# Kernel optimization log

Measured on AMD Instinct MI355X. Metric: run time of the kernel, lower is better.

Reference implementation:

```python
import jax, jax.numpy as jnp
import numpy as np
from jax import lax

B, S, D, H, K, FF = 8, 1024, 512, 8, 3, 1024
BUCKETS, MAX_REL = 32, 128
DH = D // H
SPAN = BUCKETS  # att_span when position_buckets > 0


def setup_inputs() -> dict:
    key = jax.random.key(0)
    ks = jax.random.split(key, 12)
    n = lambda k, shp, s=0.02: jax.random.normal(k, shp, jnp.float32) * s
    return dict(
        x=jax.random.normal(ks[0], (B, S, D), jnp.float32),
        ln1_g=jnp.ones((D,), jnp.float32), ln1_b=jnp.zeros((D,), jnp.float32),
        dw_w=n(ks[1], (D, 1, K), 0.1), dw_b=jnp.zeros((D,), jnp.float32),
        pw_w=n(ks[2], (D, D)), pw_b=jnp.zeros((D,), jnp.float32),
        ln2_g=jnp.ones((D,), jnp.float32), ln2_b=jnp.zeros((D,), jnp.float32),
        q_w=n(ks[3], (D, D)), q_b=jnp.zeros((D,), jnp.float32),
        k_w=n(ks[4], (D, D)), k_b=jnp.zeros((D,), jnp.float32),
        v_w=n(ks[5], (D, D)), v_b=jnp.zeros((D,), jnp.float32),
        o_w=n(ks[6], (D, D)), o_b=jnp.zeros((D,), jnp.float32),
        rel_emb=n(ks[7], (2 * SPAN, D)),
        ln3_g=jnp.ones((D,), jnp.float32), ln3_b=jnp.zeros((D,), jnp.float32),
        w1=n(ks[8], (FF, D)), b1=jnp.zeros((FF,), jnp.float32),
        w2=n(ks[9], (D, FF)), b2=jnp.zeros((D,), jnp.float32),
    )


def _ln(x, g, b):
    m = x.mean(-1, keepdims=True)
    v = jnp.var(x, axis=-1, keepdims=True)
    return (x - m) * lax.rsqrt(v + 1e-5) * g + b


def _rel_bucket():
    # DeBERTa-v2 log-bucket relative positions, [S, S] int32
    ids = jnp.arange(S, dtype=jnp.int32)
    rel = ids[:, None] - ids[None, :]
    mid = BUCKETS // 2
    sign = jnp.sign(rel)
    abs_pos = jnp.where((rel < mid) & (rel > -mid), mid - 1, jnp.abs(rel)).astype(jnp.float32)
    log_pos = jnp.ceil(jnp.log(abs_pos / mid) / np.log((MAX_REL - 1) / mid) * (mid - 1)) + mid
    return jnp.where(abs_pos <= mid, rel, (log_pos * sign).astype(jnp.int32)).astype(jnp.int32)


def _attention(x, q_w, q_b, k_w, k_b, v_w, v_b, o_w, o_b, rel_emb):
    def heads(t):  # [B,S,D] -> [B,H,S,DH]
        return t.reshape(B, S, H, DH).transpose(0, 2, 1, 3)

    q = heads(x @ q_w.T + q_b)
    k = heads(x @ k_w.T + k_b)
    v = heads(x @ v_w.T + v_b)
    scale = 1.0 / np.sqrt(DH * 3)  # scale_factor = 1 + len(['c2p','p2c'])

    scores = jnp.einsum('bhid,bhjd->bhij', q, k) * scale  # content-to-content

    rel = _rel_bucket()  # [S,S]
    # shared att key: project rel embeddings with same q/k projections -> [H, 2*SPAN, DH]
    pos_k = (rel_emb @ k_w.T + k_b).reshape(2 * SPAN, H, DH).transpose(1, 0, 2)
    pos_q = (rel_emb @ q_w.T + q_b).reshape(2 * SPAN, H, DH).transpose(1, 0, 2)

    # content-to-position
    c2p = jnp.einsum('bhid,hjd->bhij', q, pos_k)  # [B,H,S,2*SPAN]
    c2p_idx = jnp.clip(rel + SPAN, 0, 2 * SPAN - 1)[None, None]  # [1,1,S,S]
    scores = scores + jnp.take_along_axis(c2p, c2p_idx, axis=-1) * scale

    # position-to-content
    p2c = jnp.einsum('bhid,hjd->bhij', k, pos_q)  # [B,H,S,2*SPAN]
    p2c_idx = jnp.clip(-rel + SPAN, 0, 2 * SPAN - 1)[None, None]
    scores = scores + jnp.take_along_axis(p2c, p2c_idx, axis=-1).swapaxes(-1, -2) * scale

    probs = jax.nn.softmax(scores, axis=-1)
    ctx = jnp.einsum('bhij,bhjd->bhid', probs, v).transpose(0, 2, 1, 3).reshape(B, S, D)
    return ctx @ o_w.T + o_b


def reference(x, ln1_g, ln1_b, dw_w, dw_b, pw_w, pw_b, ln2_g, ln2_b,
              q_w, q_b, k_w, k_b, v_w, v_b, o_w, o_b, rel_emb,
              ln3_g, ln3_b, w1, b1, w2, b2):
    # conv block (pre-norm)
    res = x
    xn = _ln(x, ln1_g, ln1_b)
    xc = xn.transpose(0, 2, 1)  # [B,D,S]
    dw = lax.conv_general_dilated(xc, dw_w, (1,), [(K // 2, K // 2)],
                                  dimension_numbers=('NCH', 'OIH', 'NCH'),
                                  feature_group_count=D) + dw_b[None, :, None]
    pw = jnp.einsum('od,bds->bos', pw_w, jax.nn.silu(dw)) + pw_b[None, :, None]
    x = res + pw.transpose(0, 2, 1)
    # attention block
    res = x
    x = res + _attention(_ln(x, ln2_g, ln2_b), q_w, q_b, k_w, k_b, v_w, v_b, o_w, o_b, rel_emb)
    # FFN block
    res = x
    xn = _ln(x, ln3_g, ln3_b)
    ff = jax.nn.silu(xn @ w1.T + b1) @ w2.T + b2
    return res + ff
```

## Files before the change

kernel.cpp:

```cpp
#include <hip/hip_runtime.h>
#include <hip/hip_bf16.h>
#include <math.h>


#define B_  8
#define S_  1024
#define D_  512
#define H_  8
#define DH_ 64
#define FF_ 1024
#define BS_ (B_*S_)
#define SCALE_ 0.07216878364f

typedef __attribute__((ext_vector_type(8))) short  short8;
typedef __attribute__((ext_vector_type(4))) short  short4v;
typedef __attribute__((ext_vector_type(4))) float  f32x4;
typedef __attribute__((ext_vector_type(4))) int    int4v;

static __device__ __forceinline__ float b2f(short u){
  union { int i; float f; } cv; cv.i = ((int)(unsigned short)u) << 16; return cv.f;
}
static __device__ __forceinline__ short f2b(float f){
  union { float f; unsigned u; } cv; cv.f = f;
  unsigned r = cv.u + 0x7FFFu + ((cv.u >> 16) & 1u);
  return (short)(r >> 16);
}
static __device__ __forceinline__ float silu_f(float x){
  return x / (1.f + __expf(-x));
}
static __device__ __forceinline__ f32x4 mfma16(short8 a, short8 b, f32x4 c){
  return __builtin_amdgcn_mfma_f32_16x16x32_bf16(a, b, c, 0, 0, 0);
}
static __device__ __forceinline__ void gl16(const void* g, void* l){
  __builtin_amdgcn_global_load_lds((const __attribute__((address_space(1))) void*)g,
                                   (__attribute__((address_space(3))) void*)l, 16, 0, 0);
}

struct F2B8 { const float* s[8]; short* d[8]; int n[8]; };
__global__ __launch_bounds__(256) void f2b8_kernel(F2B8 a){
  int seg = blockIdx.y;
  int i = (blockIdx.x*256 + threadIdx.x)*4;
  if (i >= a.n[seg]) return;
  float4 v = *(const float4*)(a.s[seg] + i);
  short4v o; o.x = f2b(v.x); o.y = f2b(v.y); o.z = f2b(v.z); o.w = f2b(v.w);
  *(short4v*)(a.d[seg] + i) = o;
}

__global__ __launch_bounds__(256) void tab_kernel(signed char* __restrict__ tab){
  int t = blockIdx.x*256 + threadIdx.x;
  if (t >= 2048) return;
  int d = t - 1023;
  int ad = d < 0 ? -d : d;
  int bkt;
  if (ad <= 16) bkt = d;
  else {
    const float inv_log = 15.f / logf(7.9375f);
    float lp = ceilf(logf((float)ad * (1.f/16.f)) * inv_log) + 16.f;
    int ilp = (int)lp;
    bkt = (d > 0) ? ilp : -ilp;
  }
  int idx = bkt + 32;
  idx = idx < 0 ? 0 : (idx > 63 ? 63 : idx);
  tab[t] = (signed char)idx;
}

__global__ __launch_bounds__(128) void ln_kernel(const float* __restrict__ x,
                                                 const float* __restrict__ g,
                                                 const float* __restrict__ bb,
                                                 short* __restrict__ out){
  int row = blockIdx.x;
  int tid = threadIdx.x;
  float4 v = ((const float4*)(x + (size_t)row*D_))[tid];
  float s  = v.x + v.y + v.z + v.w;
  float ss = v.x*v.x + v.y*v.y + v.z*v.z + v.w*v.w;
  #pragma unroll
  for (int off = 32; off; off >>= 1){ s += __shfl_down(s, off); ss += __shfl_down(ss, off); }
  __shared__ float red[4];
  if ((tid & 63) == 0){ red[tid>>6] = s; red[2 + (tid>>6)] = ss; }
  __syncthreads();
  float S  = red[0] + red[1];
  float SS = red[2] + red[3];
  float m   = S * (1.f/D_);
  float var = SS * (1.f/D_) - m*m;
  float rs  = rsqrtf(var + 1e-5f);
  float4 gv = ((const float4*)g)[tid];
  float4 bv = ((const float4*)bb)[tid];
  short4v o;
  o.x = f2b((v.x - m)*rs*gv.x + bv.x);
  o.y = f2b((v.y - m)*rs*gv.y + bv.y);
  o.z = f2b((v.z - m)*rs*gv.z + bv.z);
  o.w = f2b((v.w - m)*rs*gv.w + bv.w);
  *(short4v*)(out + (size_t)row*D_ + tid*4) = o;
}

__global__ __launch_bounds__(256) void dwconv_kernel(const short* __restrict__ xn,
                                                     const float* __restrict__ w,
                                                     const float* __restrict__ bias,
                                                     short* __restrict__ out){
  int idx = blockIdx.x*256 + threadIdx.x;
  int bs  = idx >> 6;
  int d8  = (idx & 63) << 3;
  int s   = bs & (S_-1);
  const short* base = xn + (size_t)bs*D_ + d8;
  short8 z = {};
  short8 xm = (s > 0)     ? *(const short8*)(base - D_) : z;
  short8 xc =               *(const short8*)(base);
  short8 xp = (s < S_-1)  ? *(const short8*)(base + D_) : z;
  short8 o;
  #pragma unroll
  for (int i = 0; i < 8; i++){
    int d = d8 + i;
    float acc = bias[d] + b2f(xm[i])*w[d*3+0] + b2f(xc[i])*w[d*3+1] + b2f(xp[i])*w[d*3+2];
    o[i] = f2b(silu_f(acc));
  }
  *(short8*)(out + (size_t)bs*D_ + d8) = o;
}

#define GEMM_GL_CORE(AP, WP, KK)                                               \
  __shared__ short a_lds[128*64];                                              \
  __shared__ short b_lds[64*64];                                               \
  int tid = threadIdx.x;                                                       \
  int w = tid >> 6, lane = tid & 63, quad = lane >> 4, l16 = lane & 15;        \
  int wm = (w >> 1) * 64, wn = (w & 1) * 32;                                   \
  int m0 = blockIdx.x * 128, n0 = blockIdx.y * 64;                             \
  const short* aptr[4]; const short* bptr[2];                                  \
  _Pragma("unroll")                                                            \
  for (int i = 0; i < 4; i++){                                                 \
    int slot = i*256 + tid;                                                    \
    int r = slot >> 3, c = (slot & 7) ^ (r & 7);                               \
    aptr[i] = AP + (size_t)(m0 + r)*KK + c*8;                                  \
  }                                                                            \
  _Pragma("unroll")                                                            \
  for (int i = 0; i < 2; i++){                                                 \
    int slot = i*256 + tid;                                                    \
    int r = slot >> 3, c = (slot & 7) ^ (r & 7);                               \
    bptr[i] = WP + (size_t)(n0 + r)*KK + c*8;                                  \
  }                                                                            \
  f32x4 acc[4][2] = {};                                                        \
  int sw = l16 & 7;                                                            \
  for (int kk = 0; kk < KK; kk += 64){                                         \
    _Pragma("unroll")                                                          \
    for (int i = 0; i < 4; i++) gl16(aptr[i] + kk, &a_lds[(i*256 + w*64)*8]);  \
    _Pragma("unroll")                                                          \
    for (int i = 0; i < 2; i++) gl16(bptr[i] + kk, &b_lds[(i*256 + w*64)*8]);  \
    __syncthreads();                                                           \
    _Pragma("unroll")                                                          \
    for (int ks = 0; ks < 2; ks++){                                            \
      short8 b0 = *(const short8*)&b_lds[(wn      + l16)*64 + ((ks*4+quad)^sw)*8]; \
      short8 b1 = *(const short8*)&b_lds[(wn + 16 + l16)*64 + ((ks*4+quad)^sw)*8]; \
      _Pragma("unroll")                                                        \
      for (int mt = 0; mt < 4; mt++){                                          \
        short8 a = *(const short8*)&a_lds[(wm + mt*16 + l16)*64 + ((ks*4+quad)^sw)*8]; \
        acc[mt][0] = mfma16(a, b0, acc[mt][0]);                                \
        acc[mt][1] = mfma16(a, b1, acc[mt][1]);                                \
      }                                                                        \
    }                                                                          \
    __syncthreads();                                                           \
  }

template<bool SILU, bool RES, bool OF32, bool OBF>
__global__ __launch_bounds__(256) void gemm_gl(const short* __restrict__ A,
                                               const short* __restrict__ W,
                                               const float* __restrict__ bias,
                                               const float* res,
                                               float* of32,
                                               short* __restrict__ obf,
                                               int M, int N, int K){
  GEMM_GL_CORE(A, W, K)
  #pragma unroll
  for (int mt = 0; mt < 4; mt++)
    #pragma unroll
    for (int nt = 0; nt < 2; nt++)
      #pragma unroll
      for (int r = 0; r < 4; r++){
        int row = m0 + wm + mt*16 + quad*4 + r;
        int col = n0 + wn + nt*16 + l16;
        float val = acc[mt][nt][r] + bias[col];
        if (SILU) val = silu_f(val);
        if (RES)  val += res[(size_t)row*N + col];
        if (OF32) of32[(size_t)row*N + col] = val;
        if (OBF)  obf[(size_t)row*N + col] = f2b(val);
      }
}

__global__ __launch_bounds__(256) void gemm_qkv(const short* __restrict__ A,
                                                const short* __restrict__ W,
                                                const float* __restrict__ qb,
                                                const float* __restrict__ kb,
                                                const float* __restrict__ vb,
                                                short* __restrict__ Qo,
                                                short* __restrict__ Ko,
                                                short* __restrict__ Vo,
                                                int M, int K){
  GEMM_GL_CORE(A, W, K)
  int colb = n0 + wn;
  int sel = colb >> 9;
  const float* bp = sel == 0 ? qb : (sel == 1 ? kb : vb);
  short* dp = sel == 0 ? Qo : (sel == 1 ? Ko : Vo);
  float mult = sel == 0 ? SCALE_ : 1.f;
  #pragma unroll
  for (int mt = 0; mt < 4; mt++)
    #pragma unroll
    for (int nt = 0; nt < 2; nt++)
      #pragma unroll
      for (int r = 0; r < 4; r++){
        int row = m0 + wm + mt*16 + quad*4 + r;
        int col = (colb + nt*16 + l16) & 511;
        float val = (acc[mt][nt][r] + bp[col]) * mult;
        dp[(size_t)row*D_ + col] = f2b(val);
      }
}

__global__ __launch_bounds__(256) void gemm_pos(const short* __restrict__ A,
                                                const short* __restrict__ W,
                                                const float* __restrict__ bias,
                                                short* __restrict__ obf,
                                                float mult, int N, int K){
  __shared__ short a_lds[64][72];
  __shared__ short b_lds[64][72];
  int tid = threadIdx.x;
  int w = tid >> 6, lane = tid & 63, quad = lane >> 4, l16 = lane & 15;
  int wm = (w >> 1) * 32, wn = (w & 1) * 32;
  int m0 = 0, n0 = blockIdx.x * 64;
  int r0 = tid >> 3, c0 = (tid & 7) * 8;
  int r1 = r0 + 32;
  f32x4 acc[2][2] = {};
  for (int kk = 0; kk < K; kk += 64){
    *(int4v*)&a_lds[r0][c0] = *(const int4v*)(A + (size_t)(m0+r0)*K + kk + c0);
    *(int4v*)&a_lds[r1][c0] = *(const int4v*)(A + (size_t)(m0+r1)*K + kk + c0);
    *(int4v*)&b_lds[r0][c0] = *(const int4v*)(W + (size_t)(n0+r0)*K + kk + c0);
    *(int4v*)&b_lds[r1][c0] = *(const int4v*)(W + (size_t)(n0+r1)*K + kk + c0);
    __syncthreads();
    #pragma unroll
    for (int ks = 0; ks < 2; ks++){
      short8 a0 = *(const short8*)&a_lds[wm      + l16][ks*32 + quad*8];
      short8 a1 = *(const short8*)&a_lds[wm + 16 + l16][ks*32 + quad*8];
      short8 b0 = *(const short8*)&b_lds[wn      + l16][ks*32 + quad*8];
      short8 b1 = *(const short8*)&b_lds[wn + 16 + l16][ks*32 + quad*8];
      acc[0][0] = mfma16(a0, b0, acc[0][0]);
      acc[0][1] = mfma16(a0, b1, acc[0][1]);
      acc[1][0] = mfma16(a1, b0, acc[1][0]);
      acc[1][1] = mfma16(a1, b1, acc[1][1]);
    }
    __syncthreads();
  }
  #pragma unroll
  for (int mt = 0; mt < 2; mt++)
    #pragma unroll
    for (int nt = 0; nt < 2; nt++)
      #pragma unroll
      for (int r = 0; r < 4; r++){
        int row = m0 + wm + mt*16 + quad*4 + r;
        int col = n0 + wn + nt*16 + l16;
        obf[(size_t)row*N + col] = f2b((acc[mt][nt][r] + bias[col]) * mult);
      }
}

__global__ __launch_bounds__(256) void posbias_kernel(const short* __restrict__ q,
                                                      const short* __restrict__ k,
                                                      const short* __restrict__ posk,
                                                      const short* __restrict__ posq,
                                                      short* __restrict__ c2p,
                                                      short* __restrict__ p2c){
  int bsT = blockIdx.x;
  int h   = blockIdx.y;
  int tid = threadIdx.x, w = tid >> 6, lane = tid & 63, quad = lane >> 4, l16 = lane & 15;
  int row_a = bsT*64 + w*16 + l16;
  f32x4 accc[4] = {}, accp[4] = {};
  #pragma unroll
  for (int ks = 0; ks < 2; ks++){
    short8 aq = *(const short8*)(q + (size_t)row_a*D_ + h*DH_ + ks*32 + quad*8);
    short8 ak = *(const short8*)(k + (size_t)row_a*D_ + h*DH_ + ks*32 + quad*8);
    #pragma unroll
    for (int nt = 0; nt < 4; nt++){
      short8 bk = *(const short8*)(posk + (size_t)(nt*16+l16)*D_ + h*DH_ + ks*32 + quad*8);
      short8 bq = *(const short8*)(posq + (size_t)(nt*16+l16)*D_ + h*DH_ + ks*32 + quad*8);
      accc[nt] = mfma16(aq, bk, accc[nt]);
      accp[nt] = mfma16(ak, bq, accp[nt]);
    }
  }
  #pragma unroll
  for (int nt = 0; nt < 4; nt++)
    #pragma unroll
    for (int r = 0; r < 4; r++){
      int row = bsT*64 + w*16 + quad*4 + r;
      int col = h*DH_ + nt*16 + l16;
      c2p[(size_t)row*D_ + col] = f2b(accc[nt][r]);
      p2c[(size_t)row*D_ + col] = f2b(accp[nt][r]);
    }
}

__global__ __launch_bounds__(256) void vtrans_kernel(const short* __restrict__ v,
                                                     short* __restrict__ vt){
  __shared__ short t_lds[64][65];
  int st = blockIdx.x, h = blockIdx.y, b = blockIdx.z;
  int s0 = st*64;
  int tid = threadIdx.x;
  #pragma unroll
  for (int i = 0; i < 2; i++){
    int c = i*256 + tid;
    int s = c >> 3, d8 = (c & 7) * 8;
    short8 vv = *(const short8*)(v + (size_t)(b*S_ + s0 + s)*D_ + h*DH_ + d8);
    #pragma unroll
    for (int jj = 0; jj < 8; jj++) t_lds[d8+jj][s] = vv[jj];
  }
  __syncthreads();
  #pragma unroll
  for (int i = 0; i < 2; i++){
    int c = i*256 + tid;
    int d = c >> 3, s8 = (c & 7) * 8;
    short8 o;
    #pragma unroll
    for (int jj = 0; jj < 8; jj++) o[jj] = t_lds[d][s8+jj];
    *(short8*)(vt + ((size_t)(b*H_ + h)*DH_ + d)*S_ + s0 + s8) = o;
  }
}

#define PPS 68
__global__ __launch_bounds__(256, 4) void flash_kernel(const short* __restrict__ q,
                                                       const short* __restrict__ k,
                                                       const short* __restrict__ VT,
                                                       const short* __restrict__ c2p,
                                                       const short* __restrict__ p2c,
                                                       const signed char* __restrict__ TAB,
                                                       short* __restrict__ ctx){
  __shared__ short k_lds[64][72];
  __shared__ short v_lds[64][72];
  __shared__ short c2p_lds[64][72];
  __shared__ short pp_lds[64][PPS];
  __shared__ signed char tab[2048];

  int bh = blockIdx.x, it = blockIdx.y;
  int b = bh >> 3, h = bh & 7;
  int i0 = it * 64;
  int tid = threadIdx.x, w = tid >> 6, lane = tid & 63, quad = lane >> 4, l16 = lane & 15;

  ((unsigned long long*)tab)[tid] = ((const unsigned long long*)TAB)[tid];
  #pragma unroll
  for (int i = 0; i < 2; i++){
    int c = i*256 + tid;
    int r = c >> 3, cc = (c & 7) * 8;
    *(int4v*)&c2p_lds[r][cc] = *(const int4v*)(c2p + (size_t)(b*S_ + i0 + r)*D_ + h*DH_ + cc);
  }
  short8 qf0, qf1;
  {
    size_t row = (size_t)(b*S_ + i0 + w*16 + l16);
    qf0 = *(const short8*)(q + row*D_ + h*DH_ +      quad*8);
    qf1 = *(const short8*)(q + row*D_ + h*DH_ + 32 + quad*8);
  }
  __syncthreads();

  float cpos[4], cneg[4];
  #pragma unroll
  for (int r = 0; r < 4; r++){
    int iloc = w*16 + quad*4 + r;
    cpos[r] = b2f(c2p_lds[iloc][63]);
    cneg[r] = b2f(c2p_lds[iloc][0]);
  }
  f32x4 o_acc[4] = {};
  float lrow[4] = {};
  const short* Kbase  = k   + (size_t)(b*S_)*D_ + h*DH_;
  const short* VTbase = VT  + (size_t)(b*H_ + h)*DH_*S_;
  const short* Pbase  = p2c + (size_t)(b*S_)*D_ + h*DH_;

  int st_r = tid >> 3, st_c = (tid & 7) * 8;

  for (int jt = 0; jt < 16; jt++){
    int j0 = jt * 64;
    bool near = (jt >= it-2 && jt <= it+2);
    #pragma unroll
    for (int i = 0; i < 2; i++){
      int r = st_r + i*32;
      *(int4v*)&k_lds[r][st_c]  = *(const int4v*)(Kbase + (size_t)(j0 + r)*D_ + st_c);
      *(int4v*)&v_lds[r][st_c]  = *(const int4v*)(VTbase + (size_t)r*S_ + j0 + st_c);
      *(int4v*)&pp_lds[r][st_c] = *(const int4v*)(Pbase + (size_t)(j0 + r)*D_ + st_c);
    }
    __syncthreads();

    f32x4 sfr[4];
    #pragma unroll
    for (int nt = 0; nt < 4; nt++){
      f32x4 a = {};
      a = mfma16(qf0, *(const short8*)&k_lds[nt*16+l16][     quad*8], a);
      a = mfma16(qf1, *(const short8*)&k_lds[nt*16+l16][32 + quad*8], a);
      sfr[nt] = a;
    }
    float pval[4][4];
    if (near){
      #pragma unroll
      for (int nt = 0; nt < 4; nt++){
        int jloc = nt*16 + l16;
        #pragma unroll
        for (int r = 0; r < 4; r++){
          int iloc = w*16 + quad*4 + r;
          int idx  = tab[(i0 + iloc) - (j0 + jloc) + 1023];
          float p = __expf(sfr[nt][r] + b2f(c2p_lds[iloc][idx]) + b2f(pp_lds[jloc][idx]));
          pval[nt][r] = p;
          lrow[r] += p;
        }
      }
    } else {
      int cidx = (jt < it) ? 63 : 0;
      const float* cP = (jt < it) ? cpos : cneg;
      #pragma unroll
      for (int nt = 0; nt < 4; nt++){
        float pv = b2f(pp_lds[nt*16 + l16][cidx]);
        #pragma unroll
        for (int r = 0; r < 4; r++){
          float p = __expf(sfr[nt][r] + cP[r] + pv);
          pval[nt][r] = p;
          lrow[r] += p;
        }
      }
    }
    __syncthreads();

    #pragma unroll
    for (int nt = 0; nt < 4; nt++)
      #pragma unroll
      for (int r = 0; r < 4; r++)
        pp_lds[w*16 + quad*4 + r][nt*16 + l16] = f2b(pval[nt][r]);
    short8 pf0 = *(const short8*)&pp_lds[w*16 + l16][     quad*8];
    short8 pf1 = *(const short8*)&pp_lds[w*16 + l16][32 + quad*8];
    #pragma unroll
    for (int nt = 0; nt < 4; nt++){
      o_acc[nt] = mfma16(pf0, *(const short8*)&v_lds[nt*16+l16][     quad*8], o_acc[nt]);
      o_acc[nt] = mfma16(pf1, *(const short8*)&v_lds[nt*16+l16][32 + quad*8], o_acc[nt]);
    }
    __syncthreads();
  }
  #pragma unroll
  for (int r = 0; r < 4; r++){
    #pragma unroll
    for (int off = 8; off; off >>= 1) lrow[r] += __shfl_xor(lrow[r], off);
  }
  #pragma unroll
  for (int nt = 0; nt < 4; nt++)
    #pragma unroll
    for (int r = 0; r < 4; r++){
      size_t row = (size_t)(b*S_ + i0 + w*16 + quad*4 + r);
      ctx[row*D_ + h*DH_ + nt*16 + l16] = f2b(o_acc[nt][r] / lrow[r]);
    }
}

static const size_t OFF_XN   = 0;
static const size_t OFF_Q    = 8388608;
static const size_t OFF_K    = 16777216;
static const size_t OFF_V    = 25165824;
static const size_t OFF_C2P  = 33554432;
static const size_t OFF_P2C  = 41943040;
static const size_t OFF_WPW  = 50331648;
static const size_t OFF_WQ   = 50855936;
static const size_t OFF_WK   = 51380224;
static const size_t OFF_WV   = 51904512;
static const size_t OFF_WO   = 52428800;
static const size_t OFF_W1   = 52953088;
static const size_t OFF_W2   = 54001664;
static const size_t OFF_REL  = 55050240;
static const size_t OFF_POSK = 55115776;
static const size_t OFF_POSQ = 55181312;
static const size_t OFF_TAB  = 55246848;

extern "C" void kernel_launch(void* const* d_in, const int* in_sizes, int n_in,
                              void* d_out, int out_size, void* d_ws, size_t ws_size,
                              hipStream_t stream){
  const float* x    = (const float*)d_in[0];
  const float* ln1g = (const float*)d_in[1];
  const float* ln1b = (const float*)d_in[2];
  const float* dww  = (const float*)d_in[3];
  const float* dwb  = (const float*)d_in[4];
  const float* pww  = (const float*)d_in[5];
  const float* pwb  = (const float*)d_in[6];
  const float* ln2g = (const float*)d_in[7];
  const float* ln2b = (const float*)d_in[8];
  const float* qw   = (const float*)d_in[9];
  const float* qb   = (const float*)d_in[10];
  const float* kw   = (const float*)d_in[11];
  const float* kb   = (const float*)d_in[12];
  const float* vw   = (const float*)d_in[13];
  const float* vb   = (const float*)d_in[14];
  const float* ow   = (const float*)d_in[15];
  const float* ob   = (const float*)d_in[16];
  const float* rel  = (const float*)d_in[17];
  const float* ln3g = (const float*)d_in[18];
  const float* ln3b = (const float*)d_in[19];
  const float* w1   = (const float*)d_in[20];
  const float* b1   = (const float*)d_in[21];
  const float* w2   = (const float*)d_in[22];
  const float* b2   = (const float*)d_in[23];
  float* out = (float*)d_out;
  char* ws = (char*)d_ws;

  short* XN   = (short*)(ws + OFF_XN);
  short* Q    = (short*)(ws + OFF_Q);
  short* Kb_  = (short*)(ws + OFF_K);
  short* V    = (short*)(ws + OFF_V);
  short* C2P  = (short*)(ws + OFF_C2P);
  short* P2C  = (short*)(ws + OFF_P2C);
  short* WPW  = (short*)(ws + OFF_WPW);
  short* WQ   = (short*)(ws + OFF_WQ);
  short* WK   = (short*)(ws + OFF_WK);
  short* WV   = (short*)(ws + OFF_WV);
  short* WO   = (short*)(ws + OFF_WO);
  short* W1B  = (short*)(ws + OFF_W1);
  short* W2B  = (short*)(ws + OFF_W2);
  short* RELB = (short*)(ws + OFF_REL);
  short* POSK = (short*)(ws + OFF_POSK);
  short* POSQ = (short*)(ws + OFF_POSQ);
  signed char* TAB = (signed char*)(ws + OFF_TAB);
  short* DWS  = C2P;
  short* VT   = XN;
  short* CTX  = V;
  short* FFH  = Q;

  F2B8 fa;
  fa.s[0]=pww; fa.d[0]=WPW; fa.n[0]=262144;
  fa.s[1]=qw;  fa.d[1]=WQ;  fa.n[1]=262144;
  fa.s[2]=kw;  fa.d[2]=WK;  fa.n[2]=262144;
  fa.s[3]=vw;  fa.d[3]=WV;  fa.n[3]=262144;
  fa.s[4]=ow;  fa.d[4]=WO;  fa.n[4]=262144;
  fa.s[5]=w1;  fa.d[5]=W1B; fa.n[5]=524288;
  fa.s[6]=w2;  fa.d[6]=W2B; fa.n[6]=524288;
  fa.s[7]=rel; fa.d[7]=RELB;fa.n[7]=32768;
  f2b8_kernel<<<dim3(512,8), 256, 0, stream>>>(fa);
  tab_kernel<<<8, 256, 0, stream>>>(TAB);

  ln_kernel<<<BS_, 128, 0, stream>>>(x, ln1g, ln1b, XN);
  dwconv_kernel<<<2048, 256, 0, stream>>>(XN, dww, dwb, DWS);
  gemm_gl<false,true,true,false><<<dim3(64,8), 256, 0, stream>>>(
      DWS, WPW, pwb, x, out, nullptr, BS_, 512, 512);

  ln_kernel<<<BS_, 128, 0, stream>>>(out, ln2g, ln2b, XN);
  gemm_qkv<<<dim3(64,24), 256, 0, stream>>>(
      XN, WQ, qb, kb, vb, Q, Kb_, V, BS_, 512);
  gemm_pos<<<8, 256, 0, stream>>>(RELB, WK, kb, POSK, 1.f,    512, 512);
  gemm_pos<<<8, 256, 0, stream>>>(RELB, WQ, qb, POSQ, SCALE_, 512, 512);
  posbias_kernel<<<dim3(128,8), 256, 0, stream>>>(Q, Kb_, POSK, POSQ, C2P, P2C);
  vtrans_kernel<<<dim3(16,8,8), 256, 0, stream>>>(V, VT);
  flash_kernel<<<dim3(64,16), 256, 0, stream>>>(Q, Kb_, VT, C2P, P2C, TAB, CTX);
  gemm_gl<false,true,true,false><<<dim3(64,8), 256, 0, stream>>>(
      CTX, WO, ob, out, out, nullptr, BS_, 512, 512);

  ln_kernel<<<BS_, 128, 0, stream>>>(out, ln3g, ln3b, XN);
  gemm_gl<true,false,false,true><<<dim3(64,16), 256, 0, stream>>>(
      XN, W1B, b1, nullptr, nullptr, FFH, BS_, 1024, 512);
  gemm_gl<false,true,true,false><<<dim3(64,8), 256, 0, stream>>>(
      FFH, W2B, b2, out, out, nullptr, BS_, 512, 1024);
}
```

Measured before the change: 325.7 us.

## Double-buffer GEMM LDS loads and restructure flash tile loading with far p2c columns

The shared GEMM core now double-buffers its A/B LDS tiles, prefetching the next K slice with direct global-to-LDS loads while MFMAs run on the current one, which drops one barrier per iteration. The flash kernel loads K and V tiles via gl16 into swizzled unpadded LDS and fetches p2c tiles only for near blocks. Far blocks read a compact per-head column (p2c columns 0 and 63) that posbias now writes to a new workspace buffer. This cuts global traffic and barriers in attention, at the cost of extra LDS, an extra small output, and more delicate barrier ordering.

```diff
diff --git a/kernel.cpp b/kernel.cpp
--- a/kernel.cpp
+++ b/kernel.cpp
@@ -117,45 +117,49 @@
 }
 
 #define GEMM_GL_CORE(AP, WP, KK)                                               \
-  __shared__ short a_lds[128*64];                                              \
-  __shared__ short b_lds[64*64];                                               \
+  __shared__ short a_lds[2][128*64];                                           \
+  __shared__ short b_lds[2][64*64];                                            \
   int tid = threadIdx.x;                                                       \
   int w = tid >> 6, lane = tid & 63, quad = lane >> 4, l16 = lane & 15;        \
   int wm = (w >> 1) * 64, wn = (w & 1) * 32;                                   \
   int m0 = blockIdx.x * 128, n0 = blockIdx.y * 64;                             \
-  const short* aptr[4]; const short* bptr[2];                                  \
+  int lr = lane >> 3, lc8 = ((lane & 7) ^ lr) * 8;                             \
+  const short* asrc[4]; const short* bsrc[2];                                  \
   _Pragma("unroll")                                                            \
-  for (int i = 0; i < 4; i++){                                                 \
-    int slot = i*256 + tid;                                                    \
-    int r = slot >> 3, c = (slot & 7) ^ (r & 7);                               \
-    aptr[i] = AP + (size_t)(m0 + r)*KK + c*8;                                  \
-  }                                                                            \
+  for (int i = 0; i < 4; i++)                                                  \
+    asrc[i] = AP + (size_t)(m0 + w*32 + i*8 + lr)*KK + lc8;                    \
   _Pragma("unroll")                                                            \
-  for (int i = 0; i < 2; i++){                                                 \
-    int slot = i*256 + tid;                                                    \
-    int r = slot >> 3, c = (slot & 7) ^ (r & 7);                               \
-    bptr[i] = WP + (size_t)(n0 + r)*KK + c*8;                                  \
-  }                                                                            \
+  for (int i = 0; i < 2; i++)                                                  \
+    bsrc[i] = WP + (size_t)(n0 + w*16 + i*8 + lr)*KK + lc8;                    \
   f32x4 acc[4][2] = {};                                                        \
-  int sw = l16 & 7;                                                            \
+  int sx = l16 & 7;                                                            \
+  _Pragma("unroll")                                                            \
+  for (int i = 0; i < 4; i++) gl16(asrc[i], &a_lds[0][(w*32 + i*8)*64]);       \
+  _Pragma("unroll")                                                            \
+  for (int i = 0; i < 2; i++) gl16(bsrc[i], &b_lds[0][(w*16 + i*8)*64]);       \
+  int cur = 0;                                                                 \
   for (int kk = 0; kk < KK; kk += 64){                                         \
-    _Pragma("unroll")                                                          \
-    for (int i = 0; i < 4; i++) gl16(aptr[i] + kk, &a_lds[(i*256 + w*64)*8]);  \
-    _Pragma("unroll")                                                          \
-    for (int i = 0; i < 2; i++) gl16(bptr[i] + kk, &b_lds[(i*256 + w*64)*8]);  \
     __syncthreads();                                                           \
+    if (kk + 64 < KK){                                                         \
+      _Pragma("unroll")                                                        \
+      for (int i = 0; i < 4; i++)                                              \
+        gl16(asrc[i] + kk + 64, &a_lds[cur^1][(w*32 + i*8)*64]);               \
+      _Pragma("unroll")                                                        \
+      for (int i = 0; i < 2; i++)                                              \
+        gl16(bsrc[i] + kk + 64, &b_lds[cur^1][(w*16 + i*8)*64]);               \
+    }                                                                          \
     _Pragma("unroll")                                                          \
     for (int ks = 0; ks < 2; ks++){                                            \
-      short8 b0 = *(const short8*)&b_lds[(wn      + l16)*64 + ((ks*4+quad)^sw)*8]; \
-      short8 b1 = *(const short8*)&b_lds[(wn + 16 + l16)*64 + ((ks*4+quad)^sw)*8]; \
+      short8 b0 = *(const short8*)&b_lds[cur][((wn      + l16)<<6) + (((ks*4+quad)^sx)<<3)]; \
+      short8 b1 = *(const short8*)&b_lds[cur][((wn + 16 + l16)<<6) + (((ks*4+quad)^sx)<<3)]; \
       _Pragma("unroll")                                                        \
       for (int mt = 0; mt < 4; mt++){                                          \
-        short8 a = *(const short8*)&a_lds[(wm + mt*16 + l16)*64 + ((ks*4+quad)^sw)*8]; \
+        short8 a = *(const short8*)&a_lds[cur][((wm + mt*16 + l16)<<6) + (((ks*4+quad)^sx)<<3)]; \
         acc[mt][0] = mfma16(a, b0, acc[mt][0]);                                \
         acc[mt][1] = mfma16(a, b1, acc[mt][1]);                                \
       }                                                                        \
     }                                                                          \
-    __syncthreads();                                                           \
+    cur ^= 1;                                                                  \
   }
 
 template<bool SILU, bool RES, bool OF32, bool OBF>
@@ -261,7 +265,8 @@
                                                       const short* __restrict__ posk,
                                                       const short* __restrict__ posq,
                                                       short* __restrict__ c2p,
-                                                      short* __restrict__ p2c){
+                                                      short* __restrict__ p2c,
+                                                      short* __restrict__ pfar){
   int bsT = blockIdx.x;
   int h   = blockIdx.y;
   int tid = threadIdx.x, w = tid >> 6, lane = tid & 63, quad = lane >> 4, l16 = lane & 15;
@@ -285,8 +290,15 @@
     for (int r = 0; r < 4; r++){
       int row = bsT*64 + w*16 + quad*4 + r;
       int col = h*DH_ + nt*16 + l16;
+      short pv = f2b(accp[nt][r]);
       c2p[(size_t)row*D_ + col] = f2b(accc[nt][r]);
-      p2c[(size_t)row*D_ + col] = f2b(accp[nt][r]);
+      p2c[(size_t)row*D_ + col] = pv;
+      int cin = nt*16 + l16;
+      if (cin == 0 || cin == 63){
+        int b  = row >> 10, s = row & 1023;
+        int bh = b*H_ + h;
+        pfar[(size_t)bh*2048 + (cin ? 1024 : 0) + s] = pv;
+      }
     }
 }
 
@@ -322,10 +334,11 @@
                                                        const short* __restrict__ VT,
                                                        const short* __restrict__ c2p,
                                                        const short* __restrict__ p2c,
+                                                       const short* __restrict__ PFAR,
                                                        const signed char* __restrict__ TAB,
                                                        short* __restrict__ ctx){
-  __shared__ short k_lds[64][72];
-  __shared__ short v_lds[64][72];
+  __shared__ short k_lds[64*64];
+  __shared__ short v_lds[64*64];
   __shared__ short c2p_lds[64][72];
   __shared__ short pp_lds[64][PPS];
   __shared__ signed char tab[2048];
@@ -348,6 +361,22 @@
     qf0 = *(const short8*)(q + row*D_ + h*DH_ +      quad*8);
     qf1 = *(const short8*)(q + row*D_ + h*DH_ + 32 + quad*8);
   }
+  const short* Kbase  = k   + (size_t)(b*S_)*D_ + h*DH_;
+  const short* VTbase = VT  + (size_t)(b*H_ + h)*DH_*S_;
+  const short* Pbase  = p2c + (size_t)(b*S_)*D_ + h*DH_;
+  const short* Fbase  = PFAR + (size_t)bh*2048;
+
+  int lr = lane >> 3, lc8 = ((lane & 7) ^ lr) * 8;
+  const short* ksrc[2]; const short* vsrc[2];
+  #pragma unroll
+  for (int i = 0; i < 2; i++){
+    int rr = w*16 + i*8 + lr;
+    ksrc[i] = Kbase  + (size_t)rr*D_ + lc8;
+    vsrc[i] = VTbase + (size_t)rr*S_ + lc8;
+  }
+  int sx = l16 & 7;
+  int st_r = tid >> 3, st_c = (tid & 7) * 8;
+
   __syncthreads();
 
   float cpos[4], cneg[4];
@@ -359,30 +388,34 @@
   }
   f32x4 o_acc[4] = {};
   float lrow[4] = {};
-  const short* Kbase  = k   + (size_t)(b*S_)*D_ + h*DH_;
-  const short* VTbase = VT  + (size_t)(b*H_ + h)*DH_*S_;
-  const short* Pbase  = p2c + (size_t)(b*S_)*D_ + h*DH_;
-
-  int st_r = tid >> 3, st_c = (tid & 7) * 8;
 
   for (int jt = 0; jt < 16; jt++){
     int j0 = jt * 64;
     bool near = (jt >= it-2 && jt <= it+2);
+    int4v ppv0, ppv1;
+    if (near){
+      ppv0 = *(const int4v*)(Pbase + (size_t)(j0 + st_r     )*D_ + st_c);
+      ppv1 = *(const int4v*)(Pbase + (size_t)(j0 + st_r + 32)*D_ + st_c);
+    }
+    __syncthreads();
     #pragma unroll
     for (int i = 0; i < 2; i++){
-      int r = st_r + i*32;
-      *(int4v*)&k_lds[r][st_c]  = *(const int4v*)(Kbase + (size_t)(j0 + r)*D_ + st_c);
-      *(int4v*)&v_lds[r][st_c]  = *(const int4v*)(VTbase + (size_t)r*S_ + j0 + st_c);
-      *(int4v*)&pp_lds[r][st_c] = *(const int4v*)(Pbase + (size_t)(j0 + r)*D_ + st_c);
+      gl16(ksrc[i] + (size_t)j0*D_, &k_lds[(w*16 + i*8)*64]);
+      gl16(vsrc[i] + j0,            &v_lds[(w*16 + i*8)*64]);
+    }
+    if (near){
+      *(int4v*)&pp_lds[st_r     ][st_c] = ppv0;
+      *(int4v*)&pp_lds[st_r + 32][st_c] = ppv1;
     }
     __syncthreads();
 
     f32x4 sfr[4];
     #pragma unroll
     for (int nt = 0; nt < 4; nt++){
+      int rowb = (nt*16 + l16) << 6;
       f32x4 a = {};
-      a = mfma16(qf0, *(const short8*)&k_lds[nt*16+l16][     quad*8], a);
-      a = mfma16(qf1, *(const short8*)&k_lds[nt*16+l16][32 + quad*8], a);
+      a = mfma16(qf0, *(const short8*)&k_lds[rowb + ((quad^sx)<<3)], a);
+      a = mfma16(qf1, *(const short8*)&k_lds[rowb + (((quad+4)^sx)<<3)], a);
       sfr[nt] = a;
     }
     float pval[4][4];
@@ -399,12 +432,13 @@
           lrow[r] += p;
         }
       }
+      __syncthreads();
     } else {
-      int cidx = (jt < it) ? 63 : 0;
       const float* cP = (jt < it) ? cpos : cneg;
+      const short* fcol = Fbase + ((jt < it) ? 1024 : 0) + j0;
       #pragma unroll
       for (int nt = 0; nt < 4; nt++){
-        float pv = b2f(pp_lds[nt*16 + l16][cidx]);
+        float pv = b2f(fcol[nt*16 + l16]);
         #pragma unroll
         for (int r = 0; r < 4; r++){
           float p = __expf(sfr[nt][r] + cP[r] + pv);
@@ -413,7 +447,6 @@
         }
       }
     }
-    __syncthreads();
 
     #pragma unroll
     for (int nt = 0; nt < 4; nt++)
@@ -424,10 +457,10 @@
     short8 pf1 = *(const short8*)&pp_lds[w*16 + l16][32 + quad*8];
     #pragma unroll
     for (int nt = 0; nt < 4; nt++){
-      o_acc[nt] = mfma16(pf0, *(const short8*)&v_lds[nt*16+l16][     quad*8], o_acc[nt]);
-      o_acc[nt] = mfma16(pf1, *(const short8*)&v_lds[nt*16+l16][32 + quad*8], o_acc[nt]);
-    }
-    __syncthreads();
+      int rowb = (nt*16 + l16) << 6;
+      o_acc[nt] = mfma16(pf0, *(const short8*)&v_lds[rowb + ((quad^sx)<<3)], o_acc[nt]);
+      o_acc[nt] = mfma16(pf1, *(const short8*)&v_lds[rowb + (((quad+4)^sx)<<3)], o_acc[nt]);
+    }
   }
   #pragma unroll
   for (int r = 0; r < 4; r++){
@@ -460,6 +493,7 @@
 static const size_t OFF_POSK = 55115776;
 static const size_t OFF_POSQ = 55181312;
 static const size_t OFF_TAB  = 55246848;
+static const size_t OFF_PFAR = 55248896;
 
 extern "C" void kernel_launch(void* const* d_in, const int* in_sizes, int n_in,
                               void* d_out, int out_size, void* d_ws, size_t ws_size,
@@ -508,6 +542,7 @@
   short* POSK = (short*)(ws + OFF_POSK);
   short* POSQ = (short*)(ws + OFF_POSQ);
   signed char* TAB = (signed char*)(ws + OFF_TAB);
+  short* PFAR = (short*)(ws + OFF_PFAR);
   short* DWS  = C2P;
   short* VT   = XN;
   short* CTX  = V;
@@ -535,9 +570,9 @@
       XN, WQ, qb, kb, vb, Q, Kb_, V, BS_, 512);
   gemm_pos<<<8, 256, 0, stream>>>(RELB, WK, kb, POSK, 1.f,    512, 512);
   gemm_pos<<<8, 256, 0, stream>>>(RELB, WQ, qb, POSQ, SCALE_, 512, 512);
-  posbias_kernel<<<dim3(128,8), 256, 0, stream>>>(Q, Kb_, POSK, POSQ, C2P, P2C);
+  posbias_kernel<<<dim3(128,8), 256, 0, stream>>>(Q, Kb_, POSK, POSQ, C2P, P2C, PFAR);
   vtrans_kernel<<<dim3(16,8,8), 256, 0, stream>>>(V, VT);
-  flash_kernel<<<dim3(64,16), 256, 0, stream>>>(Q, Kb_, VT, C2P, P2C, TAB, CTX);
+  flash_kernel<<<dim3(64,16), 256, 0, stream>>>(Q, Kb_, VT, C2P, P2C, PFAR, TAB, CTX);
   gemm_gl<false,true,true,false><<<dim3(64,8), 256, 0, stream>>>(
       CTX, WO, ob, out, out, nullptr, BS_, 512, 512);
 
```

Result: no change. 323.2 us (-0.8%).
